# Kernel optimization log

Hardware: AMD Instinct MI355X
Metric: run time of the kernel (lower is better)

## Reference

```python
import jax, jax.numpy as jnp
import numpy as np

B, L, C, N_LAYERS, N_NBR, HID = 16, 512, 4, 4, 2, 256

def setup_inputs() -> dict:
    key = jax.random.key(0)
    k = jax.random.split(key, 5)
    n = jax.random.normal(k[0], (B, L, 3), dtype=jnp.float32)
    w_self = jnp.ones((C, N_LAYERS), dtype=jnp.float32)
    w_nbr = 0.1 * jnp.ones((C, N_LAYERS, N_NBR), dtype=jnp.float32)
    W1 = jax.random.normal(k[1], (C * L, HID), dtype=jnp.float32) * (1.0 / np.sqrt(C * L))
    b1 = jnp.zeros((HID,), dtype=jnp.float32)
    W2 = jax.random.normal(k[2], (HID, 1), dtype=jnp.float32) * (0.01 / np.sqrt(HID))
    b2 = jnp.zeros((1,), dtype=jnp.float32)
    return {"n": n, "w_self": w_self, "w_nbr": w_nbr, "W1": W1, "b1": b1, "W2": W2, "b2": b2}

def reference(n, w_self, w_nbr, W1, b1, W2, b2):
    act = jax.nn.celu
    # 1) O(3)-invariant Gram matrix, diagonal removed
    g = jnp.einsum('...id,...jd->...ij', n, n)   # (B, L, L)
    L_ = g.shape[-1]
    mask = 1.0 - jnp.eye(L_, dtype=g.dtype)
    g = g * mask
    Cc, n_layers = w_self.shape
    n_nbr = w_nbr.shape[-1]
    # (B, C, L, L)
    x = jnp.broadcast_to(g[..., None, :, :], g.shape[:-2] + (Cc, L_, L_))
    for ell in range(n_layers):
        y = w_self[:, ell][:, None, None] * x
        for d in range(1, n_nbr + 1):
            s = (jnp.roll(x, d, axis=-1) + jnp.roll(x, -d, axis=-1)
                 + jnp.roll(x, d, axis=-2) + jnp.roll(x, -d, axis=-2))
            y = y + w_nbr[:, ell, d - 1][:, None, None] * s
        x = x + act(y)
        x = 0.5 * (x + jnp.swapaxes(x, -1, -2))  # symmetrize
        x = x * mask                              # zero diagonal
    # 4) cyclic diagonal sums: c_r = sum_i x[..., i, (i+r) mod L]  (single gather)
    i = jnp.arange(L_)
    cols = (i[:, None] + i[None, :]) % L_         # (L_i, L_r)
    sep = x[..., i[:, None], cols].sum(axis=-2)   # (B, C, L)
    # 5) MLP head
    h = sep.reshape(*sep.shape[:-2], -1)          # (B, C*L)
    h = act(h @ W1 + b1)
    y = jnp.squeeze(h @ W2 + b2, axis=-1)         # (B,)
    return jnp.exp(-y)
```

## Files before the change

kernel.cpp:

```cpp
#include <hip/hip_runtime.h>

#define LSZ 512
#define CCH 4
#define NLAY 4
#define TILE 64
#define HALO 8
#define RG  80
#define RGP 82
#define NT  512

typedef float v2f __attribute__((ext_vector_type(2)));

__device__ __forceinline__ v2f pk_add(v2f a, v2f b) {
    v2f d; asm("v_pk_add_f32 %0, %1, %2" : "=v"(d) : "v"(a), "v"(b)); return d;
}
__device__ __forceinline__ v2f pk_mul(v2f a, v2f b) {
    v2f d; asm("v_pk_mul_f32 %0, %1, %2" : "=v"(d) : "v"(a), "v"(b)); return d;
}
__device__ __forceinline__ v2f pk_fma(v2f a, v2f b, v2f c) {
    v2f d; asm("v_pk_fma_f32 %0, %1, %2, %3" : "=v"(d) : "v"(a), "v"(b), "v"(c)); return d;
}
__device__ __forceinline__ v2f celu2(v2f y) {
    v2f r;
    r.x = y.x >= 0.0f ? y.x : __expf(y.x) - 1.0f;
    r.y = y.y >= 0.0f ? y.y : __expf(y.y) - 1.0f;
    return r;
}
__device__ __forceinline__ v2f ld2(const float* p) { return *(const v2f*)p; }

__device__ __forceinline__ int weights_uniform(const float* __restrict__ w_self,
                                               const float* __restrict__ w_nbr)
{
    const int lane = threadIdx.x & 63;
    bool ok = true;
    if (lane < 12) {
        int c = 1 + lane / 4, e = lane % 4;
        ok = (w_self[c * 4 + e] == w_self[e]);
    } else if (lane < 36) {
        int u = lane - 12;
        int c = 1 + u / 8, r = u % 8;
        ok = (w_nbr[c * 8 + r] == w_nbr[r]);
    }
    unsigned long long vote = __ballot(ok);
    return vote == ~0ull ? 1 : 0;
}

__global__ __launch_bounds__(NT, 4) void stencil_kernel(
    const float* __restrict__ nn,
    const float* __restrict__ w_self,
    const float* __restrict__ w_nbr,
    float* __restrict__ sep)
{
    __shared__ __align__(16) float buf[2 * RG * RGP];
    __shared__ float nrow[RG][3];
    __shared__ float ncol[RG][3];

    const int tid = threadIdx.x;
    const int bid = blockIdx.x;
    const int b = bid / 36;
    int t = bid - b * 36;
    const int uni = weights_uniform(w_self, w_nbr);

    int ti = 0;
    while (t >= 8 - ti) { t -= 8 - ti; ti++; }
    const int tj = ti + t;
    const int gi0 = ti * TILE;
    const int gj0 = tj * TILE;
    const int dd = (gj0 - gi0) & (LSZ - 1);
    const bool tile_masked = (dd == 0) || (dd == 64) || (dd == 448);

    for (int u = tid; u < RG * 3 * 2; u += NT) {
        int which = u >= RG * 3;
        int v = which ? u - RG * 3 : u;
        int rr = v / 3, d = v - 3 * rr;
        int base = which ? gj0 : gi0;
        int gl = (base - HALO + rr) & (LSZ - 1);
        float val = nn[(b * LSZ + gl) * 3 + d];
        if (which) ncol[rr][d] = val; else nrow[rr][d] = val;
    }

    int ofs[4];
    int iv[4], jv[4];
    int ring[4];
    int ew[4];
#pragma unroll
    for (int it = 0; it < 4; it++) {
        int g = tid + NT * it;
        if (g < 1600) {
            int gi2 = g / 40;
            int i = 2 * gi2, j = 2 * (g - 40 * gi2);
            iv[it] = i; jv[it] = j;
            ofs[it]  = i * RGP + j;
            ring[it] = min(min(i, 78 - i), min(j, 78 - j));
            ew[it]   = (i - j - dd + 1) & 511;
        } else { ofs[it] = -1; iv[it] = 0; jv[it] = 0; ring[it] = -1; ew[it] = 99; }
    }
    __syncthreads();

    float* const B0 = buf;
    float* const B1 = buf + RG * RGP;
    const int nch = uni ? 1 : CCH;

    for (int cc = 0; cc < nch; cc++) {
#pragma unroll
        for (int it = 0; it < 4; it++) {
            if (ofs[it] < 0) continue;
            int i = iv[it], j = jv[it];
            float a00 = nrow[i][0],   a01 = nrow[i][1],   a02 = nrow[i][2];
            float a10 = nrow[i+1][0], a11 = nrow[i+1][1], a12 = nrow[i+1][2];
            float c00 = ncol[j][0],   c01 = ncol[j][1],   c02 = ncol[j][2];
            float c10 = ncol[j+1][0], c11 = ncol[j+1][1], c12 = ncol[j+1][2];
            float g00 = a00*c00 + a01*c01 + a02*c02;
            float g01 = a00*c10 + a01*c11 + a02*c12;
            float g10 = a10*c00 + a11*c01 + a12*c02;
            float g11 = a10*c10 + a11*c11 + a12*c12;
            if (tile_masked) {
                if (ew[it] == 1) { g00 = 0.0f; g11 = 0.0f; }
                if (ew[it] == 2)   g01 = 0.0f;
                if (ew[it] == 0)   g10 = 0.0f;
            }
            *(v2f*)&B0[ofs[it]]       = (v2f){g00, g01};
            *(v2f*)&B0[ofs[it] + RGP] = (v2f){g10, g11};
        }
        __syncthreads();

        for (int ell = 0; ell < NLAY; ell++) {
            const float wsv = w_self[cc * NLAY + ell];
            const float wn1 = w_nbr[(cc * NLAY + ell) * 2 + 0];
            const float wn2 = w_nbr[(cc * NLAY + ell) * 2 + 1];
            const v2f ws2 = (v2f){wsv, wsv};
            const v2f w12 = (v2f){wn1, wn1};
            const v2f w22 = (v2f){wn2, wn2};
            const int pad = 2 * (ell + 1);
            const float* S = (ell & 1) ? B1 : B0;
            float*       D = (ell & 1) ? B0 : B1;
#pragma unroll
            for (int it = 0; it < 4; it++) {
                if (ring[it] < pad) continue;
                const float* P = S + ofs[it];
                v2f cm2 = ld2(P - 2*RGP);
                v2f cm1 = ld2(P -   RGP);
                v2f c0  = ld2(P);
                v2f cp1 = ld2(P +   RGP);
                v2f cp2 = ld2(P + 2*RGP);
                v2f cp3 = ld2(P + 3*RGP);
                v2f A0  = ld2(P - 2);
                v2f C0  = ld2(P + 2);
                v2f A1  = ld2(P + RGP - 2);
                v2f C1  = ld2(P + RGP + 2);
                v2f s1a; s1a.x = A0.y + c0.y;  s1a.y = c0.x + C0.x;
                v2f s2a = pk_add(A0, C0);
                v2f v1a = pk_add(cm1, cp1);
                v2f v2a = pk_add(cm2, cp2);
                v2f ya = pk_fma(ws2, c0, pk_fma(w12, pk_add(s1a, v1a),
                                        pk_mul(w22, pk_add(s2a, v2a))));
                v2f s1b; s1b.x = A1.y + cp1.y; s1b.y = cp1.x + C1.x;
                v2f s2b = pk_add(A1, C1);
                v2f v1b = pk_add(c0,  cp2);
                v2f v2b = pk_add(cm1, cp3);
                v2f yb = pk_fma(ws2, cp1, pk_fma(w12, pk_add(s1b, v1b),
                                         pk_mul(w22, pk_add(s2b, v2b))));
                v2f xa = pk_add(c0,  celu2(ya));
                v2f xb = pk_add(cp1, celu2(yb));
                if (tile_masked) {
                    if (ew[it] == 1) { xa.x = 0.0f; xb.y = 0.0f; }
                    if (ew[it] == 2)   xa.y = 0.0f;
                    if (ew[it] == 0)   xb.x = 0.0f;
                }
                *(v2f*)&D[ofs[it]]       = xa;
                *(v2f*)&D[ofs[it] + RGP] = xb;
            }
            __syncthreads();
        }

        if (tid < 508) {
            int dt = tid >> 2;
            int part = tid & 3;
            int delta = dt - 63;
            int ad = delta < 0 ? -delta : delta;
            int Nd = 64 - ad;
            int i0 = 8 + (delta < 0 ? -delta : 0);
            int base = i0 * RGP + (i0 + delta);
            float s = 0.0f;
            for (int k = part; k < Nd; k += 4)
                s += B0[base + k * (RGP + 1)];
            s += __shfl_xor(s, 1);
            s += __shfl_xor(s, 2);
            if (part == 0) {
                int r = (gj0 - gi0 + delta) & (LSZ - 1);
                float* sp = sep + (b * CCH + cc) * LSZ;
                atomicAdd(sp + r, s);
                if (ti != tj)
                    atomicAdd(sp + ((LSZ - r) & (LSZ - 1)), s);
            }
        }
        if (cc + 1 < nch) __syncthreads();
    }
}

__global__ __launch_bounds__(256) void mlp1_kernel(
    const float* __restrict__ sep,
    const float* __restrict__ W1,
    const float* __restrict__ w_self,
    const float* __restrict__ w_nbr,
    float* __restrict__ partial)
{
    __shared__ float4 red[4][64];
    const int uni = weights_uniform(w_self, w_nbr);
    const int mmask = uni ? (LSZ - 1) : (CCH * LSZ - 1);
    const int b  = blockIdx.x >> 5;
    const int ms = blockIdx.x & 31;
    const int kq = threadIdx.x & 63;
    const int mq = threadIdx.x >> 6;
    const int m0 = ms * 64 + mq * 16;
    const float* sv = sep + b * (CCH * LSZ);
    const float* w  = W1 + m0 * 256 + kq * 4;
    float4 a0 = {0,0,0,0}, a1 = {0,0,0,0};
#pragma unroll
    for (int m = 0; m < 16; m += 2) {
        float4 w0 = *(const float4*)(w + (m)     * 256);
        float4 w1 = *(const float4*)(w + (m + 1) * 256);
        float s0 = sv[(m0 + m) & mmask], s1 = sv[(m0 + m + 1) & mmask];
        a0.x += s0 * w0.x; a0.y += s0 * w0.y; a0.z += s0 * w0.z; a0.w += s0 * w0.w;
        a1.x += s1 * w1.x; a1.y += s1 * w1.y; a1.z += s1 * w1.z; a1.w += s1 * w1.w;
    }
    float4 a;
    a.x = a0.x + a1.x; a.y = a0.y + a1.y; a.z = a0.z + a1.z; a.w = a0.w + a1.w;
    red[mq][kq] = a;
    __syncthreads();
    if (mq == 0) {
        float4 r0 = red[0][kq], r1 = red[1][kq], r2 = red[2][kq], r3 = red[3][kq];
        float4 o;
        o.x = (r0.x + r1.x) + (r2.x + r3.x);
        o.y = (r0.y + r1.y) + (r2.y + r3.y);
        o.z = (r0.z + r1.z) + (r2.z + r3.z);
        o.w = (r0.w + r1.w) + (r2.w + r3.w);
        *(float4*)&partial[(b * 32 + ms) * 256 + kq * 4] = o;
    }
}

__global__ __launch_bounds__(256) void mlp2_kernel(
    const float* __restrict__ partial,
    const float* __restrict__ b1,
    const float* __restrict__ W2,
    const float* __restrict__ b2,
    float* __restrict__ out)
{
    __shared__ double red[4];
    const int b = blockIdx.x;
    const int k = threadIdx.x;
    double s = 0;
#pragma unroll
    for (int p = 0; p < 32; p++)
        s += (double)partial[(b * 32 + p) * 256 + k];
    s += (double)b1[k];
    s = s >= 0.0 ? s : exp(s) - 1.0;
    double q = s * (double)W2[k];
    for (int off = 32; off >= 1; off >>= 1) q += __shfl_down(q, off);
    if ((k & 63) == 0) red[k >> 6] = q;
    __syncthreads();
    if (k == 0) {
        double y = ((red[0] + red[1]) + (red[2] + red[3])) + (double)b2[0];
        out[b] = (float)exp(-y);
    }
}

extern "C" void kernel_launch(void* const* d_in, const int* in_sizes, int n_in,
                              void* d_out, int out_size, void* d_ws, size_t ws_size,
                              hipStream_t stream) {
    const float* nn     = (const float*)d_in[0];
    const float* w_self = (const float*)d_in[1];
    const float* w_nbr  = (const float*)d_in[2];
    const float* W1     = (const float*)d_in[3];
    const float* b1     = (const float*)d_in[4];
    const float* W2     = (const float*)d_in[5];
    const float* b2     = (const float*)d_in[6];
    float* out = (float*)d_out;
    float* sep     = (float*)d_ws;
    float* partial = (float*)((char*)d_ws + 128 * 1024);

    hipMemsetAsync(sep, 0, 16 * CCH * LSZ * sizeof(float), stream);
    stencil_kernel<<<16 * 36, NT, 0, stream>>>(nn, w_self, w_nbr, sep);
    mlp1_kernel<<<512, 256, 0, stream>>>(sep, W1, w_self, w_nbr, partial);
    mlp2_kernel<<<16, 256, 0, stream>>>(partial, b1, W2, b2, out);
}
```

Baseline: 87.55 us.

## Pack two or three stencil tiles per 1024-thread block on 256 blocks

The stencil kernel now processes two or three 64x64 tiles per block, with 1024 threads over 256 blocks instead of 576 blocks of 512 threads. Each tile gets its own LDS slab. The ping-pong buffers inside a slab overlap by two halo rows to fit the budget, and masking is folded into per-element ew codes. The aim is one block per CU with even work distribution and fewer block launches. The cost is a large LDS footprint, only one block per CU, and more per-thread indexing logic.

```diff
diff --git a/kernel.cpp b/kernel.cpp
--- a/kernel.cpp
+++ b/kernel.cpp
@@ -7,7 +7,9 @@
 #define HALO 8
 #define RG  80
 #define RGP 82
-#define NT  512
+#define SLAB (156 * RGP)
+#define B1OFF (78 * RGP)
+#define NT  1024
 
 typedef float v2f __attribute__((ext_vector_type(2)));
 
@@ -51,76 +53,94 @@
     const float* __restrict__ w_nbr,
     float* __restrict__ sep)
 {
-    __shared__ __align__(16) float buf[2 * RG * RGP];
-    __shared__ float nrow[RG][3];
-    __shared__ float ncol[RG][3];
+    __shared__ __align__(16) float buf[3 * SLAB];
+    __shared__ float nrc[6][RG][3];
 
     const int tid = threadIdx.x;
     const int bid = blockIdx.x;
-    const int b = bid / 36;
-    int t = bid - b * 36;
     const int uni = weights_uniform(w_self, w_nbr);
-
-    int ti = 0;
-    while (t >= 8 - ti) { t -= 8 - ti; ti++; }
-    const int tj = ti + t;
-    const int gi0 = ti * TILE;
-    const int gj0 = tj * TILE;
-    const int dd = (gj0 - gi0) & (LSZ - 1);
-    const bool tile_masked = (dd == 0) || (dd == 64) || (dd == 448);
-
-    for (int u = tid; u < RG * 3 * 2; u += NT) {
-        int which = u >= RG * 3;
-        int v = which ? u - RG * 3 : u;
-        int rr = v / 3, d = v - 3 * rr;
-        int base = which ? gj0 : gi0;
-        int gl = (base - HALO + rr) & (LSZ - 1);
-        float val = nn[(b * LSZ + gl) * 3 + d];
-        if (which) ncol[rr][d] = val; else nrow[rr][d] = val;
-    }
-
-    int ofs[4];
-    int iv[4], jv[4];
-    int ring[4];
-    int ew[4];
-#pragma unroll
-    for (int it = 0; it < 4; it++) {
-        int g = tid + NT * it;
-        if (g < 1600) {
-            int gi2 = g / 40;
-            int i = 2 * gi2, j = 2 * (g - 40 * gi2);
-            iv[it] = i; jv[it] = j;
-            ofs[it]  = i * RGP + j;
+    const int ntl = bid < 64 ? 3 : 2;
+    const int id0 = bid < 64 ? bid * 3 : 192 + (bid - 64) * 2;
+
+    int bb0, bb1, bb2, gi0_0, gi0_1, gi0_2, gj0_0, gj0_1, gj0_2;
+    int dd0, dd1, dd2; int tm0, tm1, tm2;
+#pragma unroll
+    for (int q = 0; q < 3; q++) {
+        int id = id0 + (q < ntl ? q : 0);
+        int b = id / 36;
+        int t = id - b * 36;
+        int ti = 0;
+        while (t >= 8 - ti) { t -= 8 - ti; ti++; }
+        int tj = ti + t;
+        int gi0 = ti * TILE, gj0 = tj * TILE;
+        int dd = (gj0 - gi0) & (LSZ - 1);
+        int tm = (dd == 0) || (dd == 64) || (dd == 448);
+        if (q == 0) { bb0 = b; gi0_0 = gi0; gj0_0 = gj0; dd0 = dd; tm0 = tm; }
+        if (q == 1) { bb1 = b; gi0_1 = gi0; gj0_1 = gj0; dd1 = dd; tm1 = tm; }
+        if (q == 2) { bb2 = b; gi0_2 = gi0; gj0_2 = gj0; dd2 = dd; tm2 = tm; }
+    }
+
+    for (int u = tid; u < ntl * 480; u += NT) {
+        int q = u / 480;
+        int v = u - q * 480;
+        int which = v >= 240 ? 1 : 0;
+        int w2 = which ? v - 240 : v;
+        int rr = w2 / 3, d = w2 - 3 * rr;
+        int gb = which ? (q == 2 ? gj0_2 : (q == 1 ? gj0_1 : gj0_0))
+                       : (q == 2 ? gi0_2 : (q == 1 ? gi0_1 : gi0_0));
+        int b  = q == 2 ? bb2 : (q == 1 ? bb1 : bb0);
+        int gl = (gb - HALO + rr) & (LSZ - 1);
+        nrc[q * 2 + which][rr][d] = nn[(b * LSZ + gl) * 3 + d];
+    }
+
+    int ofs[5], ring[5], ew[5], iv[5], jv[5], tl[5];
+    const int total = ntl * 1600;
+#pragma unroll
+    for (int it = 0; it < 5; it++) {
+        int base = it * NT;
+        int rem = total - base;
+        int g = -1;
+        if (rem >= NT) g = base + tid;
+        else if (rem > 0) {
+            int per = rem >> 4;
+            int lane = tid & 63, wv = tid >> 6;
+            if (lane < per) g = base + wv * per + lane;
+        }
+        if (g >= 0) {
+            int q = g >= 3200 ? 2 : (g >= 1600 ? 1 : 0);
+            int r = g - 1600 * q;
+            int gi2 = r / 40;
+            int i = 2 * gi2, j = 2 * (r - 40 * gi2);
+            int dd = q == 2 ? dd2 : (q == 1 ? dd1 : dd0);
+            int tm = q == 2 ? tm2 : (q == 1 ? tm1 : tm0);
+            tl[it] = q; iv[it] = i; jv[it] = j;
+            ofs[it] = q * SLAB + i * RGP + j;
             ring[it] = min(min(i, 78 - i), min(j, 78 - j));
-            ew[it]   = (i - j - dd + 1) & 511;
-        } else { ofs[it] = -1; iv[it] = 0; jv[it] = 0; ring[it] = -1; ew[it] = 99; }
+            int e = (i - j - dd + 1) & 511;
+            ew[it] = tm ? e : 99;
+        } else { ofs[it] = -1; ring[it] = -1; ew[it] = 99; iv[it] = 0; jv[it] = 0; tl[it] = 0; }
     }
     __syncthreads();
 
-    float* const B0 = buf;
-    float* const B1 = buf + RG * RGP;
     const int nch = uni ? 1 : CCH;
-
     for (int cc = 0; cc < nch; cc++) {
 #pragma unroll
-        for (int it = 0; it < 4; it++) {
+        for (int it = 0; it < 5; it++) {
             if (ofs[it] < 0) continue;
-            int i = iv[it], j = jv[it];
-            float a00 = nrow[i][0],   a01 = nrow[i][1],   a02 = nrow[i][2];
-            float a10 = nrow[i+1][0], a11 = nrow[i+1][1], a12 = nrow[i+1][2];
-            float c00 = ncol[j][0],   c01 = ncol[j][1],   c02 = ncol[j][2];
-            float c10 = ncol[j+1][0], c11 = ncol[j+1][1], c12 = ncol[j+1][2];
+            int i = iv[it], j = jv[it], q2 = 2 * tl[it];
+            float a00 = nrc[q2][i][0],   a01 = nrc[q2][i][1],   a02 = nrc[q2][i][2];
+            float a10 = nrc[q2][i+1][0], a11 = nrc[q2][i+1][1], a12 = nrc[q2][i+1][2];
+            float c00 = nrc[q2+1][j][0],   c01 = nrc[q2+1][j][1],   c02 = nrc[q2+1][j][2];
+            float c10 = nrc[q2+1][j+1][0], c11 = nrc[q2+1][j+1][1], c12 = nrc[q2+1][j+1][2];
             float g00 = a00*c00 + a01*c01 + a02*c02;
             float g01 = a00*c10 + a01*c11 + a02*c12;
             float g10 = a10*c00 + a11*c01 + a12*c02;
             float g11 = a10*c10 + a11*c11 + a12*c12;
-            if (tile_masked) {
-                if (ew[it] == 1) { g00 = 0.0f; g11 = 0.0f; }
-                if (ew[it] == 2)   g01 = 0.0f;
-                if (ew[it] == 0)   g10 = 0.0f;
-            }
-            *(v2f*)&B0[ofs[it]]       = (v2f){g00, g01};
-            *(v2f*)&B0[ofs[it] + RGP] = (v2f){g10, g11};
+            if (ew[it] == 1) { g00 = 0.0f; g11 = 0.0f; }
+            if (ew[it] == 2)   g01 = 0.0f;
+            if (ew[it] == 0)   g10 = 0.0f;
+            *(v2f*)&buf[ofs[it]]       = (v2f){g00, g01};
+            *(v2f*)&buf[ofs[it] + RGP] = (v2f){g10, g11};
         }
         __syncthreads();
 
@@ -131,13 +151,14 @@
             const v2f ws2 = (v2f){wsv, wsv};
             const v2f w12 = (v2f){wn1, wn1};
             const v2f w22 = (v2f){wn2, wn2};
-            const int pad = 2 * (ell + 1);
-            const float* S = (ell & 1) ? B1 : B0;
-            float*       D = (ell & 1) ? B0 : B1;
-#pragma unroll
-            for (int it = 0; it < 4; it++) {
+            const int pad  = 2 * (ell + 1);
+            const int soff = (ell & 1) ? B1OFF : 0;
+            const int doff = (ell & 1) ? 0 : B1OFF;
+#pragma unroll
+            for (int it = 0; it < 5; it++) {
                 if (ring[it] < pad) continue;
-                const float* P = S + ofs[it];
+                const float* P = buf + ofs[it] + soff;
+                float*       D = buf + ofs[it] + doff;
                 v2f cm2 = ld2(P - 2*RGP);
                 v2f cm1 = ld2(P -   RGP);
                 v2f c0  = ld2(P);
@@ -162,35 +183,59 @@
                                          pk_mul(w22, pk_add(s2b, v2b))));
                 v2f xa = pk_add(c0,  celu2(ya));
                 v2f xb = pk_add(cp1, celu2(yb));
-                if (tile_masked) {
-                    if (ew[it] == 1) { xa.x = 0.0f; xb.y = 0.0f; }
-                    if (ew[it] == 2)   xa.y = 0.0f;
-                    if (ew[it] == 0)   xb.x = 0.0f;
-                }
-                *(v2f*)&D[ofs[it]]       = xa;
-                *(v2f*)&D[ofs[it] + RGP] = xb;
+                if (ew[it] == 1) { xa.x = 0.0f; xb.y = 0.0f; }
+                if (ew[it] == 2)   xa.y = 0.0f;
+                if (ew[it] == 0)   xb.x = 0.0f;
+                *(v2f*)&D[0]   = xa;
+                *(v2f*)&D[RGP] = xb;
             }
             __syncthreads();
         }
 
-        if (tid < 508) {
-            int dt = tid >> 2;
-            int part = tid & 3;
+        {
+            int q = -1, t0 = 0;
+            if (tid < 508) { q = 0; t0 = tid; }
+            else if (tid >= 512 && tid < 1020) { q = 1; t0 = tid - 512; }
+            if (q >= 0) {
+                int dt = t0 >> 2, part = t0 & 3;
+                int delta = dt - 63;
+                int ad = delta < 0 ? -delta : delta;
+                int Nd = 64 - ad;
+                int i0 = 8 + (delta < 0 ? -delta : 0);
+                int base = q * SLAB + i0 * RGP + (i0 + delta);
+                float s = 0.0f;
+                for (int k = part; k < Nd; k += 4)
+                    s += buf[base + k * (RGP + 1)];
+                s += __shfl_xor(s, 1);
+                s += __shfl_xor(s, 2);
+                if (part == 0) {
+                    int dd = q == 1 ? dd1 : dd0;
+                    int b  = q == 1 ? bb1 : bb0;
+                    int r = (dd + delta) & (LSZ - 1);
+                    float* sp = sep + (b * CCH + cc) * LSZ;
+                    atomicAdd(sp + r, s);
+                    if (dd != 0)
+                        atomicAdd(sp + ((LSZ - r) & (LSZ - 1)), s);
+                }
+            }
+        }
+        if (ntl == 3 && tid < 508) {
+            int dt = tid >> 2, part = tid & 3;
             int delta = dt - 63;
             int ad = delta < 0 ? -delta : delta;
             int Nd = 64 - ad;
             int i0 = 8 + (delta < 0 ? -delta : 0);
-            int base = i0 * RGP + (i0 + delta);
+            int base = 2 * SLAB + i0 * RGP + (i0 + delta);
             float s = 0.0f;
             for (int k = part; k < Nd; k += 4)
-                s += B0[base + k * (RGP + 1)];
+                s += buf[base + k * (RGP + 1)];
             s += __shfl_xor(s, 1);
             s += __shfl_xor(s, 2);
             if (part == 0) {
-                int r = (gj0 - gi0 + delta) & (LSZ - 1);
-                float* sp = sep + (b * CCH + cc) * LSZ;
+                int r = (dd2 + delta) & (LSZ - 1);
+                float* sp = sep + (bb2 * CCH + cc) * LSZ;
                 atomicAdd(sp + r, s);
-                if (ti != tj)
+                if (dd2 != 0)
                     atomicAdd(sp + ((LSZ - r) & (LSZ - 1)), s);
             }
         }
@@ -280,7 +325,7 @@
     float* partial = (float*)((char*)d_ws + 128 * 1024);
 
     hipMemsetAsync(sep, 0, 16 * CCH * LSZ * sizeof(float), stream);
-    stencil_kernel<<<16 * 36, NT, 0, stream>>>(nn, w_self, w_nbr, sep);
+    stencil_kernel<<<256, NT, 0, stream>>>(nn, w_self, w_nbr, sep);
     mlp1_kernel<<<512, 256, 0, stream>>>(sep, W1, w_self, w_nbr, partial);
     mlp2_kernel<<<16, 256, 0, stream>>>(partial, b1, W2, b2, out);
 }
```

Result: slower. 89.45 us (+2.2%).

## Use 4x4 register tiles per thread with vec4 LDS loads in stencil

Applied to the files above, without the earlier changes.

Each thread now owns a 4x4 block of the 80x80 tile instead of four 2x2 blocks, loading an 8-row column of float4s plus left/right halos. Vertical neighbours are reused across rows in registers, which cuts LDS load instructions per output. The LDS slab is padded (RGP 84, origin offset) so vec4 accesses stay aligned and halo reads stay in bounds. Only 400 of 512 threads are active, and border cells are handled by a per-element select that copies the old value, which adds register pressure and leaves some lanes idle.

```diff
diff --git a/kernel.cpp b/kernel.cpp
--- a/kernel.cpp
+++ b/kernel.cpp
@@ -6,10 +6,14 @@
 #define TILE 64
 #define HALO 8
 #define RG  80
-#define RGP 82
+#define RGP 84
+#define BROWS 84
+#define BSLAB (BROWS * RGP)
+#define ORIGIN (2 * RGP + 4)
 #define NT  512
 
 typedef float v2f __attribute__((ext_vector_type(2)));
+typedef float v4f __attribute__((ext_vector_type(4)));
 
 __device__ __forceinline__ v2f pk_add(v2f a, v2f b) {
     v2f d; asm("v_pk_add_f32 %0, %1, %2" : "=v"(d) : "v"(a), "v"(b)); return d;
@@ -27,6 +31,9 @@
     return r;
 }
 __device__ __forceinline__ v2f ld2(const float* p) { return *(const v2f*)p; }
+__device__ __forceinline__ v4f ld4(const float* p) { return *(const v4f*)p; }
+__device__ __forceinline__ v2f lo2(v4f v) { return __builtin_shufflevector(v, v, 0, 1); }
+__device__ __forceinline__ v2f hi2(v4f v) { return __builtin_shufflevector(v, v, 2, 3); }
 
 __device__ __forceinline__ int weights_uniform(const float* __restrict__ w_self,
                                                const float* __restrict__ w_nbr)
@@ -51,7 +58,7 @@
     const float* __restrict__ w_nbr,
     float* __restrict__ sep)
 {
-    __shared__ __align__(16) float buf[2 * RG * RGP];
+    __shared__ __align__(16) float buf[2 * BSLAB];
     __shared__ float nrow[RG][3];
     __shared__ float ncol[RG][3];
 
@@ -79,48 +86,42 @@
         if (which) ncol[rr][d] = val; else nrow[rr][d] = val;
     }
 
-    int ofs[4];
-    int iv[4], jv[4];
-    int ring[4];
-    int ew[4];
-#pragma unroll
-    for (int it = 0; it < 4; it++) {
-        int g = tid + NT * it;
-        if (g < 1600) {
-            int gi2 = g / 40;
-            int i = 2 * gi2, j = 2 * (g - 40 * gi2);
-            iv[it] = i; jv[it] = j;
-            ofs[it]  = i * RGP + j;
-            ring[it] = min(min(i, 78 - i), min(j, 78 - j));
-            ew[it]   = (i - j - dd + 1) & 511;
-        } else { ofs[it] = -1; iv[it] = 0; jv[it] = 0; ring[it] = -1; ew[it] = 99; }
-    }
+    const bool has = tid < 400;
+    int i = 0, j = 0;
+    if (has) { int r = tid / 20; i = 4 * r; j = 4 * (tid - 20 * r); }
+    const int OFS = ORIGIN + i * RGP + j;
+    const int e = (i - j - dd) & 511;
+    bool dm[7];
+#pragma unroll
+    for (int k = -3; k <= 3; k++) dm[k + 3] = (e == (k & 511));
     __syncthreads();
 
-    float* const B0 = buf;
-    float* const B1 = buf + RG * RGP;
     const int nch = uni ? 1 : CCH;
-
     for (int cc = 0; cc < nch; cc++) {
-#pragma unroll
-        for (int it = 0; it < 4; it++) {
-            if (ofs[it] < 0) continue;
-            int i = iv[it], j = jv[it];
-            float a00 = nrow[i][0],   a01 = nrow[i][1],   a02 = nrow[i][2];
-            float a10 = nrow[i+1][0], a11 = nrow[i+1][1], a12 = nrow[i+1][2];
-            float c00 = ncol[j][0],   c01 = ncol[j][1],   c02 = ncol[j][2];
-            float c10 = ncol[j+1][0], c11 = ncol[j+1][1], c12 = ncol[j+1][2];
-            float g00 = a00*c00 + a01*c01 + a02*c02;
-            float g01 = a00*c10 + a01*c11 + a02*c12;
-            float g10 = a10*c00 + a11*c01 + a12*c02;
-            float g11 = a10*c10 + a11*c11 + a12*c12;
-            if (tile_masked) {
-                if (ew[it] == 1) { g00 = 0.0f; g11 = 0.0f; }
-                if (ew[it] == 2)   g01 = 0.0f;
-                if (ew[it] == 0)   g10 = 0.0f;
+        if (has) {
+            float ar[4][3], cb[4][3];
+#pragma unroll
+            for (int r = 0; r < 4; r++)
+#pragma unroll
+                for (int d = 0; d < 3; d++) {
+                    ar[r][d] = nrow[i + r][d];
+                    cb[r][d] = ncol[j + r][d];
+                }
+#pragma unroll
+            for (int r = 0; r < 4; r++) {
+                float g0 = ar[r][0]*cb[0][0] + ar[r][1]*cb[0][1] + ar[r][2]*cb[0][2];
+                float g1 = ar[r][0]*cb[1][0] + ar[r][1]*cb[1][1] + ar[r][2]*cb[1][2];
+                float g2 = ar[r][0]*cb[2][0] + ar[r][1]*cb[2][1] + ar[r][2]*cb[2][2];
+                float g3 = ar[r][0]*cb[3][0] + ar[r][1]*cb[3][1] + ar[r][2]*cb[3][2];
+                if (tile_masked) {
+                    if (dm[3 - r]) g0 = 0.0f;
+                    if (dm[4 - r]) g1 = 0.0f;
+                    if (dm[5 - r]) g2 = 0.0f;
+                    if (dm[6 - r]) g3 = 0.0f;
+                }
+                v4f gv = (v4f){g0, g1, g2, g3};
+                *(v4f*)&buf[OFS + r * RGP] = gv;
             }
-            *(v2f*)&B0[ofs[it]]       = (v2f){g00, g01};
-            *(v2f*)&B0[ofs[it] + RGP] = (v2f){g10, g11};
         }
         __syncthreads();
 
@@ -131,44 +132,59 @@
             const v2f ws2 = (v2f){wsv, wsv};
             const v2f w12 = (v2f){wn1, wn1};
             const v2f w22 = (v2f){wn2, wn2};
-            const int pad = 2 * (ell + 1);
-            const float* S = (ell & 1) ? B1 : B0;
-            float*       D = (ell & 1) ? B0 : B1;
-#pragma unroll
-            for (int it = 0; it < 4; it++) {
-                if (ring[it] < pad) continue;
-                const float* P = S + ofs[it];
-                v2f cm2 = ld2(P - 2*RGP);
-                v2f cm1 = ld2(P -   RGP);
-                v2f c0  = ld2(P);
-                v2f cp1 = ld2(P +   RGP);
-                v2f cp2 = ld2(P + 2*RGP);
-                v2f cp3 = ld2(P + 3*RGP);
-                v2f A0  = ld2(P - 2);
-                v2f C0  = ld2(P + 2);
-                v2f A1  = ld2(P + RGP - 2);
-                v2f C1  = ld2(P + RGP + 2);
-                v2f s1a; s1a.x = A0.y + c0.y;  s1a.y = c0.x + C0.x;
-                v2f s2a = pk_add(A0, C0);
-                v2f v1a = pk_add(cm1, cp1);
-                v2f v2a = pk_add(cm2, cp2);
-                v2f ya = pk_fma(ws2, c0, pk_fma(w12, pk_add(s1a, v1a),
-                                        pk_mul(w22, pk_add(s2a, v2a))));
-                v2f s1b; s1b.x = A1.y + cp1.y; s1b.y = cp1.x + C1.x;
-                v2f s2b = pk_add(A1, C1);
-                v2f v1b = pk_add(c0,  cp2);
-                v2f v2b = pk_add(cm1, cp3);
-                v2f yb = pk_fma(ws2, cp1, pk_fma(w12, pk_add(s1b, v1b),
-                                         pk_mul(w22, pk_add(s2b, v2b))));
-                v2f xa = pk_add(c0,  celu2(ya));
-                v2f xb = pk_add(cp1, celu2(yb));
-                if (tile_masked) {
-                    if (ew[it] == 1) { xa.x = 0.0f; xb.y = 0.0f; }
-                    if (ew[it] == 2)   xa.y = 0.0f;
-                    if (ew[it] == 0)   xb.x = 0.0f;
+            const int p = 2 * (ell + 1);
+            const int rlo = max(0, p - i), rhi = min(3, 79 - p - i);
+            const int clo = max(0, p - j), chi = min(3, 79 - p - j);
+            const bool act = has && (rlo <= rhi) && (clo <= chi);
+            const float* S = buf + ((ell & 1) ? BSLAB : 0) + OFS;
+            float*       D = buf + ((ell & 1) ? 0 : BSLAB) + OFS;
+            if (act) {
+                bool cok[4];
+#pragma unroll
+                for (int c = 0; c < 4; c++) cok[c] = (c >= clo) && (c <= chi);
+                v4f V[8];
+#pragma unroll
+                for (int k = 0; k < 8; k++) V[k] = ld4(S + (k - 2) * RGP);
+                v2f L[4], R[4];
+#pragma unroll
+                for (int r = 0; r < 4; r++) {
+                    L[r] = ld2(S + r * RGP - 2);
+                    R[r] = ld2(S + r * RGP + 4);
                 }
-                *(v2f*)&D[ofs[it]]       = xa;
-                *(v2f*)&D[ofs[it] + RGP] = xb;
+#pragma unroll
+                for (int r = 0; r < 4; r++) {
+                    v2f c0 = lo2(V[r + 2]);
+                    v2f c1 = hi2(V[r + 2]);
+                    v2f s1a; s1a.x = L[r].y + c0.y; s1a.y = c0.x + c1.x;
+                    v2f s2a = pk_add(L[r], c1);
+                    v2f v1a = pk_add(lo2(V[r + 1]), lo2(V[r + 3]));
+                    v2f v2a = pk_add(lo2(V[r]),     lo2(V[r + 4]));
+                    v2f ya = pk_fma(ws2, c0, pk_fma(w12, pk_add(s1a, v1a),
+                                            pk_mul(w22, pk_add(s2a, v2a))));
+                    v2f xa = pk_add(c0, celu2(ya));
+                    v2f s1b; s1b.x = c0.y + c1.y; s1b.y = c1.x + R[r].x;
+                    v2f s2b = pk_add(c0, R[r]);
+                    v2f v1b = pk_add(hi2(V[r + 1]), hi2(V[r + 3]));
+                    v2f v2b = pk_add(hi2(V[r]),     hi2(V[r + 4]));
+                    v2f yb = pk_fma(ws2, c1, pk_fma(w12, pk_add(s1b, v1b),
+                                            pk_mul(w22, pk_add(s2b, v2b))));
+                    v2f xb = pk_add(c1, celu2(yb));
+                    float xn0 = xa.x, xn1 = xa.y, xn2 = xb.x, xn3 = xb.y;
+                    if (tile_masked) {
+                        if (dm[3 - r]) xn0 = 0.0f;
+                        if (dm[4 - r]) xn1 = 0.0f;
+                        if (dm[5 - r]) xn2 = 0.0f;
+                        if (dm[6 - r]) xn3 = 0.0f;
+                    }
+                    const bool rok = (r >= rlo) && (r <= rhi);
+                    v4f cur = V[r + 2];
+                    v4f o;
+                    o.x = (rok && cok[0]) ? xn0 : cur.x;
+                    o.y = (rok && cok[1]) ? xn1 : cur.y;
+                    o.z = (rok && cok[2]) ? xn2 : cur.z;
+                    o.w = (rok && cok[3]) ? xn3 : cur.w;
+                    *(v4f*)&D[r * RGP] = o;
+                }
             }
             __syncthreads();
         }
@@ -180,10 +196,10 @@
             int ad = delta < 0 ? -delta : delta;
             int Nd = 64 - ad;
             int i0 = 8 + (delta < 0 ? -delta : 0);
-            int base = i0 * RGP + (i0 + delta);
+            int base = ORIGIN + i0 * RGP + (i0 + delta);
             float s = 0.0f;
             for (int k = part; k < Nd; k += 4)
-                s += B0[base + k * (RGP + 1)];
+                s += buf[base + k * (RGP + 1)];
             s += __shfl_xor(s, 1);
             s += __shfl_xor(s, 2);
             if (part == 0) {
```

Measured after the change: 89.51 us. 1.02x slower.

## Replace atomic diagonal-sum accumulation with per-tile partials reduced in MLP kernel

Applied to the files above, without the earlier changes.

The stencil kernel now writes each tile's 127 diagonal sums to its own slot in a per-tile partial buffer instead of doing global atomicAdds into sep. This also removes the memset that zeroed sep. The first MLP kernel gathers, for each of its 64 sep entries, the matching partials across all 36 tiles into shared memory before the GEMV. The goal is to drop the memset launch and atomic contention. The cost is a serial 36-tile gather loop of scattered global loads at the start of every MLP block.

```diff
diff --git a/kernel.cpp b/kernel.cpp
--- a/kernel.cpp
+++ b/kernel.cpp
@@ -49,7 +49,7 @@
     const float* __restrict__ nn,
     const float* __restrict__ w_self,
     const float* __restrict__ w_nbr,
-    float* __restrict__ sep)
+    float* __restrict__ tpart)
 {
     __shared__ __align__(16) float buf[2 * RG * RGP];
     __shared__ float nrow[RG][3];
@@ -59,6 +59,7 @@
     const int bid = blockIdx.x;
     const int b = bid / 36;
     int t = bid - b * 36;
+    const int tlin = t;
     const int uni = weights_uniform(w_self, w_nbr);
 
     int ti = 0;
@@ -183,29 +184,25 @@
             int base = i0 * RGP + (i0 + delta);
             float s = 0.0f;
             for (int k = part; k < Nd; k += 4)
-                s += B0[base + k * (RGP + 1)];
+                s += buf[base + k * (RGP + 1)];
             s += __shfl_xor(s, 1);
             s += __shfl_xor(s, 2);
-            if (part == 0) {
-                int r = (gj0 - gi0 + delta) & (LSZ - 1);
-                float* sp = sep + (b * CCH + cc) * LSZ;
-                atomicAdd(sp + r, s);
-                if (ti != tj)
-                    atomicAdd(sp + ((LSZ - r) & (LSZ - 1)), s);
-            }
+            if (part == 0)
+                tpart[((b * CCH + cc) * 36 + tlin) * 128 + dt] = s;
         }
         if (cc + 1 < nch) __syncthreads();
     }
 }
 
 __global__ __launch_bounds__(256) void mlp1_kernel(
-    const float* __restrict__ sep,
+    const float* __restrict__ tpart,
     const float* __restrict__ W1,
     const float* __restrict__ w_self,
     const float* __restrict__ w_nbr,
     float* __restrict__ partial)
 {
     __shared__ float4 red[4][64];
+    __shared__ float sepL[64];
     const int uni = weights_uniform(w_self, w_nbr);
     const int mmask = uni ? (LSZ - 1) : (CCH * LSZ - 1);
     const int b  = blockIdx.x >> 5;
@@ -213,14 +210,39 @@
     const int kq = threadIdx.x & 63;
     const int mq = threadIdx.x >> 6;
     const int m0 = ms * 64 + mq * 16;
-    const float* sv = sep + b * (CCH * LSZ);
-    const float* w  = W1 + m0 * 256 + kq * 4;
+
+    if (threadIdx.x < 64) {
+        int u = threadIdx.x;
+        int B = (ms * 64 + u) & mmask;
+        int cc = B >> 9;
+        int r  = B & (LSZ - 1);
+        const float* tp = tpart + (b * CCH + cc) * 36 * 128;
+        float acc = 0.0f;
+        int t = 0;
+        for (int ti = 0; ti < 8; ti++) {
+            for (int tj = ti; tj < 8; tj++, t++) {
+                int dd = ((tj - ti) * TILE) & (LSZ - 1);
+                int d1 = (r - dd) & (LSZ - 1);
+                if (d1 <= 63)       acc += tp[t * 128 + d1 + 63];
+                else if (d1 >= 449) acc += tp[t * 128 + d1 - 449];
+                if (ti != tj) {
+                    int d2 = (-r - dd) & (LSZ - 1);
+                    if (d2 <= 63)       acc += tp[t * 128 + d2 + 63];
+                    else if (d2 >= 449) acc += tp[t * 128 + d2 - 449];
+                }
+            }
+        }
+        sepL[u] = acc;
+    }
+    __syncthreads();
+
+    const float* w = W1 + m0 * 256 + kq * 4;
     float4 a0 = {0,0,0,0}, a1 = {0,0,0,0};
 #pragma unroll
     for (int m = 0; m < 16; m += 2) {
         float4 w0 = *(const float4*)(w + (m)     * 256);
         float4 w1 = *(const float4*)(w + (m + 1) * 256);
-        float s0 = sv[(m0 + m) & mmask], s1 = sv[(m0 + m + 1) & mmask];
+        float s0 = sepL[mq * 16 + m], s1 = sepL[mq * 16 + m + 1];
         a0.x += s0 * w0.x; a0.y += s0 * w0.y; a0.z += s0 * w0.z; a0.w += s0 * w0.w;
         a1.x += s1 * w1.x; a1.y += s1 * w1.y; a1.z += s1 * w1.z; a1.w += s1 * w1.w;
     }
@@ -276,11 +298,10 @@
     const float* W2     = (const float*)d_in[5];
     const float* b2     = (const float*)d_in[6];
     float* out = (float*)d_out;
-    float* sep     = (float*)d_ws;
-    float* partial = (float*)((char*)d_ws + 128 * 1024);
-
-    hipMemsetAsync(sep, 0, 16 * CCH * LSZ * sizeof(float), stream);
-    stencil_kernel<<<16 * 36, NT, 0, stream>>>(nn, w_self, w_nbr, sep);
-    mlp1_kernel<<<512, 256, 0, stream>>>(sep, W1, w_self, w_nbr, partial);
+    float* tpart   = (float*)d_ws;
+    float* partial = (float*)((char*)d_ws + 1216 * 1024);
+
+    stencil_kernel<<<16 * 36, NT, 0, stream>>>(nn, w_self, w_nbr, tpart);
+    mlp1_kernel<<<512, 256, 0, stream>>>(tpart, W1, w_self, w_nbr, partial);
     mlp2_kernel<<<16, 256, 0, stream>>>(partial, b1, W2, b2, out);
 }
```

After: 95.49 us. 1.09x slower.
